# Kernel optimization log

Measured on AMD Instinct MI355X. Metric: run time of the kernel, lower is better.

The kernel has to match this reference:

```python
import jax, jax.numpy as jnp
import numpy as np

RES_UP_RATIO = 0.05   # reserve_up_ratio (mgr.args default)
RES_DN_RATIO = 0.02   # reserve_dn_ratio
REQ_UP_RATIO = 0.02   # system_reserve_up_ratio
REQ_DN_RATIO = 0.02   # system_reserve_dn_ratio


def _build_K(G):
    """Static constraint matrix of the per-timestep LP over x=[P, R_up, R_dn] (n=3G).
    Row 0 is the equality sum(P)=D; remaining rows are <= inequalities."""
    n = 3 * G
    m = 1 + 4 * G + 2
    K = np.zeros((m, n), dtype=np.float32)
    I = np.eye(G, dtype=np.float32)
    K[0, :G] = 1.0                      # sum_g P = D
    r = 1
    K[r:r+G, :G] = I;  K[r:r+G, G:2*G] = I;  r += G      # P + R_up <= pmax
    K[r:r+G, :G] = -I; K[r:r+G, 2*G:3*G] = I; r += G     # -P + R_dn <= -pmin
    K[r:r+G, :G] = I;  r += G                             # P <= pmax
    K[r:r+G, :G] = -I; r += G                             # -P <= -pmin
    K[r, G:2*G] = -1.0; r += 1                            # -sum R_up <= -req_up*D
    K[r, 2*G:3*G] = -1.0                                  # -sum R_dn <= -req_dn*D
    return K


def _solve_da_lp(forecast, pmin, pmax, b, n_iters):
    """Batched PDHG (Chambolle-Pock) solve of all B*T per-timestep LPs.
    Returns P, R_up, R_dn with shape (B, T, G)."""
    B, T = forecast.shape
    G = b.shape[0]
    Knp = _build_K(G)
    L = float(np.linalg.norm(Knp, 2))          # static spectral norm of K
    tau = sigma = 0.9 / L
    K = jnp.asarray(Knp)
    m, n = K.shape
    # objective coefficients over x=[P, R_up, R_dn] (Cost = b*P + c is affine)
    c_obj = jnp.concatenate([b, RES_UP_RATIO * b, RES_DN_RATIO * b])  # (n,)
    # rhs q: (B, T, m)
    q = jnp.concatenate([
        forecast[..., None],
        jnp.broadcast_to(pmax, (B, T, G)),
        jnp.broadcast_to(-pmin, (B, T, G)),
        jnp.broadcast_to(pmax, (B, T, G)),
        jnp.broadcast_to(-pmin, (B, T, G)),
        -REQ_UP_RATIO * forecast[..., None],
        -REQ_DN_RATIO * forecast[..., None],
    ], axis=-1)
    ineq = (jnp.arange(m) > 0)  # row 0 = equality dual (unprojected)

    x0 = jnp.zeros((B, T, n), dtype=forecast.dtype)
    y0 = jnp.zeros((B, T, m), dtype=forecast.dtype)

    def step(carry, _):
        x, y = carry
        x_new = jnp.maximum(x - tau * (c_obj + jnp.einsum('btm,mn->btn', y, K)), 0.0)
        x_bar = 2.0 * x_new - x
        y_new = y + sigma * (jnp.einsum('btn,mn->btm', x_bar, K) - q)
        y_new = jnp.where(ineq, jnp.maximum(y_new, 0.0), y_new)
        return (x_new, y_new), None

    (x, _), _ = jax.lax.scan(step, (x0, y0), None, length=n_iters)
    P = x[..., :G]
    Ru = x[..., G:2*G]
    Rd = x[..., 2*G:3*G]
    return P, Ru, Rd


def setup_inputs() -> dict:
    key = jax.random.key(0)
    k1, k2, k3, k4 = jax.random.split(key, 4)
    G, B, T = 50, 128, 24
    pmax = 100.0 + 400.0 * jax.random.uniform(k1, (G,), dtype=jnp.float32)
    pmin = 0.1 * pmax
    b = 20.0 + 30.0 * jax.random.uniform(k2, (G,), dtype=jnp.float32)
    c = 100.0 * jax.random.uniform(k3, (G,), dtype=jnp.float32)
    lo, hi = jnp.sum(pmin), jnp.sum(pmax)
    # feasible demand: comfortably inside [sum pmin, sum pmax] so reserves exist
    forecast = lo + (0.35 + 0.3 * jax.random.uniform(k4, (B, T), dtype=jnp.float32)) * (hi - lo)
    return {"forecast": forecast, "pmin": pmin, "pmax": pmax, "b": b, "c": c, "n_iters": 300}


def reference(forecast, pmin, pmax, b, c, n_iters):
    P, Ru, Rd = _solve_da_lp(forecast, pmin, pmax, b, n_iters)  # (B,T,G)
    # match torch layout (B, G, T)
    P_DA = jnp.swapaxes(P, 1, 2)
    R_up = jnp.swapaxes(Ru, 1, 2)
    R_dn = jnp.swapaxes(Rd, 1, 2)
    Cost_DA = b[None, :, None] * P_DA + c[None, :, None]
    ru_price = (RES_UP_RATIO * b)[None, :, None]
    rd_price = (RES_DN_RATIO * b)[None, :, None]
    obj = Cost_DA.sum((1, 2)) + (ru_price * R_up).sum((1, 2)) + (rd_price * R_dn).sum((1, 2))
    return (P_DA, R_up, R_dn, obj, Cost_DA)
```

## Files before the change

### kernel.cpp

```cpp
#include <hip/hip_runtime.h>
#include <math.h>

#define G   50
#define T   24
#define B   128
#define NLP (B * T)
#define SZ  (B * G * T)

typedef float v2f __attribute__((ext_vector_type(2)));


__device__ __forceinline__ v2f vmax0(v2f v) {
    v2f z = {0.f, 0.f};
    return __builtin_elementwise_max(v, z);
}

template <int CTRL>
__device__ __forceinline__ float dpp_mov(float x) {
    int r = __builtin_amdgcn_update_dpp(0, __float_as_int(x), CTRL, 0xf, 0xf, true);
    return __int_as_float(r);
}

__device__ __forceinline__ void row_sum3(float& a, float& b, float& c) {
    asm("s_nop 1\n\t"
        "v_add_f32_dpp %0, %0, %0 row_ror:1 row_mask:0xf bank_mask:0xf\n\t"
        "v_add_f32_dpp %1, %1, %1 row_ror:1 row_mask:0xf bank_mask:0xf\n\t"
        "v_add_f32_dpp %2, %2, %2 row_ror:1 row_mask:0xf bank_mask:0xf\n\t"
        "v_add_f32_dpp %0, %0, %0 row_ror:2 row_mask:0xf bank_mask:0xf\n\t"
        "v_add_f32_dpp %1, %1, %1 row_ror:2 row_mask:0xf bank_mask:0xf\n\t"
        "v_add_f32_dpp %2, %2, %2 row_ror:2 row_mask:0xf bank_mask:0xf\n\t"
        "v_add_f32_dpp %0, %0, %0 row_ror:4 row_mask:0xf bank_mask:0xf\n\t"
        "v_add_f32_dpp %1, %1, %1 row_ror:4 row_mask:0xf bank_mask:0xf\n\t"
        "v_add_f32_dpp %2, %2, %2 row_ror:4 row_mask:0xf bank_mask:0xf\n\t"
        "v_add_f32_dpp %0, %0, %0 row_ror:8 row_mask:0xf bank_mask:0xf\n\t"
        "v_add_f32_dpp %1, %1, %1 row_ror:8 row_mask:0xf bank_mask:0xf\n\t"
        "v_add_f32_dpp %2, %2, %2 row_ror:8 row_mask:0xf bank_mask:0xf"
        : "+v"(a), "+v"(b), "+v"(c));
}

__device__ __forceinline__ float row_sum1(float a) {
    a += dpp_mov<0x121>(a);
    a += dpp_mov<0x122>(a);
    a += dpp_mov<0x124>(a);
    a += dpp_mov<0x128>(a);
    return a;
}

__device__ __forceinline__ float half_sum1(float a) {
    a = row_sum1(a);
    float t;
    asm("ds_swizzle_b32 %0, %1 offset:0x401f\n\t"
        "s_waitcnt lgkmcnt(0)"
        : "=&v"(t) : "v"(a));
    return a + t;
}

__global__ __launch_bounds__(64)
void pdhg_lp_kernel(const float* __restrict__ forecast,
                    const float* __restrict__ pmin,
                    const float* __restrict__ pmax,
                    const float* __restrict__ bcost,
                    const float* __restrict__ ccost,
                    const int*   __restrict__ n_iters_p,
                    float* __restrict__ out,
                    float* __restrict__ ws_partial,
                    float tau)
{
    const int lane = threadIdx.x;
    const int l    = lane & 31;
    const int half = lane >> 5;
    const int lp   = blockIdx.x * 2 + half;
    const int b    = lp / T;
    const int t    = lp - b * T;
    const int n_iters = n_iters_p[0];

    const int  g0 = l;
    const int  g1 = l + 32;
    const bool v1 = (l < 18);

    v2f bj  = { bcost[g0], v1 ? bcost[g1] : 0.f };
    v2f cj  = { ccost[g0], v1 ? ccost[g1] : 0.f };
    v2f pmx = { pmax[g0],  v1 ? pmax[g1]  : 0.f };
    v2f pmn = { pmin[g0],  v1 ? pmin[g1]  : 0.f };
    const float f = forecast[lp];

    const float ts  = tau * tau;
    const float BIG = 1e30f;

    v2f tcP  = tau * bj;           if (!v1) tcP.y  = BIG;
    v2f tcRu = (tau * 0.05f) * bj; if (!v1) tcRu.y = BIG;
    v2f tcRd = (tau * 0.02f) * bj; if (!v1) tcRd.y = BIG;
    v2f tspmx = ts * pmx, tspmn = ts * pmn;
    const float tsf   = ts * f;
    const float tsreq = ts * 0.02f * f;

    v2f P = {0,0}, Ru = {0,0}, Rd = {0,0};
    v2f z1 = {0,0}, z2 = {0,0}, z3 = {0,0}, z4 = {0,0};
    float z0 = 0.f, zru = 0.f, zrd = 0.f;

    for (int it = 0; it < n_iters; ++it) {
        v2f z0v  = { z0,  z0  };
        v2f zruv = { zru, zru };
        v2f zrdv = { zrd, zrd };
        v2f gP  = (z1 - z2) + (z3 - z4) + z0v;
        v2f Pn  = vmax0(P  - tcP  - gP);
        v2f Run = vmax0(Ru - tcRu - z1 + zruv);
        v2f Rdn = vmax0(Rd - tcRd - z2 + zrdv);

        v2f Pb  = 2.f * Pn  - P;
        v2f Rub = 2.f * Run - Ru;
        v2f Rdb = 2.f * Rdn - Rd;
        P = Pn; Ru = Run; Rd = Rdn;

        float sP  = Pb.x  + Pb.y;
        float sRu = Rub.x + Rub.y;
        float sRd = Rdb.x + Rdb.y;
        row_sum3(sP, sRu, sRd);

        float xP, xRu, xRd;
        asm("ds_swizzle_b32 %0, %3 offset:0x401f\n\t"
            "ds_swizzle_b32 %1, %4 offset:0x401f\n\t"
            "ds_swizzle_b32 %2, %5 offset:0x401f"
            : "=&v"(xP), "=&v"(xRu), "=&v"(xRd)
            : "v"(sP), "v"(sRu), "v"(sRd));

        z1 = vmax0(z1 + ts * (Pb + Rub) - tspmx);
        z2 = vmax0(z2 + ts * (Rdb - Pb) + tspmn);
        z3 = vmax0(z3 + ts * Pb - tspmx);
        z4 = vmax0(z4 - ts * Pb + tspmn);

        asm("s_waitcnt lgkmcnt(0)" : "+v"(xP), "+v"(xRu), "+v"(xRd));
        sP += xP; sRu += xRu; sRd += xRd;

        z0  = z0 + ts * sP - tsf;
        zru = fmaxf(zru + tsreq - ts * sRu, 0.f);
        zrd = fmaxf(zrd + tsreq - ts * sRd, 0.f);
    }

    const v2f cost = bj * P + cj;
    {
        const int bgt = b * (G * T) + t;
        const int a0 = bgt + g0 * T;
        out[a0] = P.x;  out[SZ + a0] = Ru.x;  out[2*SZ + a0] = Rd.x;  out[3*SZ + B + a0] = cost.x;
        if (v1) {
            const int a1 = bgt + g1 * T;
            out[a1] = P.y;  out[SZ + a1] = Ru.y;  out[2*SZ + a1] = Rd.y;  out[3*SZ + B + a1] = cost.y;
        }
    }

    if (ws_partial) {
        v2f lo = cost + (0.05f * bj) * Ru + (0.02f * bj) * Rd;
        float tot = half_sum1(lo.x + lo.y);
        if (l == 0) ws_partial[lp] = tot;
    }
}

__global__ __launch_bounds__(64)
void obj_final_kernel(const float* __restrict__ ws_partial, float* __restrict__ out)
{
    const int b = blockIdx.x * 64 + threadIdx.x;
    if (b < B) {
        float s = 0.f;
        #pragma unroll
        for (int t = 0; t < T; ++t) s += ws_partial[b * T + t];
        out[3 * SZ + b] = s;
    }
}

__global__ __launch_bounds__(256)
void obj_kernel(const float* __restrict__ bcost, float* __restrict__ out)
{
    const int b = blockIdx.x;
    const float* Ru = out + SZ     + (size_t)b * (G * T);
    const float* Rd = out + 2 * SZ + (size_t)b * (G * T);
    const float* C  = out + 3 * SZ + B + (size_t)b * (G * T);

    float s = 0.f;
    for (int i = threadIdx.x; i < G * T; i += 256) {
        const int g = i / T;
        const float bg = bcost[g];
        s += C[i] + 0.05f * bg * Ru[i] + 0.02f * bg * Rd[i];
    }
    __shared__ float sm[16];
    s = row_sum1(s);
    if ((threadIdx.x & 15) == 0) sm[threadIdx.x >> 4] = s;
    __syncthreads();
    if (threadIdx.x == 0) {
        float tot = 0.f;
        #pragma unroll
        for (int i = 0; i < 16; ++i) tot += sm[i];
        out[3 * SZ + b] = tot;
    }
}

extern "C" void kernel_launch(void* const* d_in, const int* in_sizes, int n_in,
                              void* d_out, int out_size, void* d_ws, size_t ws_size,
                              hipStream_t stream) {
    const float* forecast = (const float*)d_in[0];
    const float* pmin_p   = (const float*)d_in[1];
    const float* pmax_p   = (const float*)d_in[2];
    const float* b_p      = (const float*)d_in[3];
    const float* c_p      = (const float*)d_in[4];
    const int*   niter_p  = (const int*)  d_in[5];
    float* out = (float*)d_out;

    const double L = sqrt((105.0 + sqrt(17.0)) * 0.5);
    const float tau = (float)(0.9 / L);

    const bool use_ws = (ws_size >= (size_t)NLP * sizeof(float));
    float* wsp = use_ws ? (float*)d_ws : nullptr;

    pdhg_lp_kernel<<<NLP / 2, 64, 0, stream>>>(forecast, pmin_p, pmax_p,
                                               b_p, c_p, niter_p, out, wsp, tau);
    if (use_ws) {
        obj_final_kernel<<<(B + 63) / 64, 64, 0, stream>>>(wsp, out);
    } else {
        obj_kernel<<<B, 256, 0, stream>>>(b_p, out);
    }
}
```

Measured before the change: 147.2 us.

## Map one LP per wavefront with full-wave DPP reduction and readlane

Switches from packing two LPs per 64-lane wavefront, with two generators per lane held in float2 vectors, to one LP per wavefront with one generator per lane. Only 50 of the 64 lanes do useful work. The per-iteration sums now use row_bcast DPP steps plus v_readlane into scalar registers, replacing the ds_swizzle exchange that went through the LDS unit and needed a wait on it. The grid doubles, which gives more waves per SIMD to hide the latency of the serial 300-iteration loop. The cost is more total VALU instructions and fewer lanes doing useful work.

```diff
diff --git a/kernel.cpp b/kernel.cpp
--- a/kernel.cpp
+++ b/kernel.cpp
@@ -7,13 +7,6 @@
 #define NLP (B * T)
 #define SZ  (B * G * T)
 
-typedef float v2f __attribute__((ext_vector_type(2)));
-
-
-__device__ __forceinline__ v2f vmax0(v2f v) {
-    v2f z = {0.f, 0.f};
-    return __builtin_elementwise_max(v, z);
-}
 
 template <int CTRL>
 __device__ __forceinline__ float dpp_mov(float x) {
@@ -21,7 +14,16 @@
     return __int_as_float(r);
 }
 
-__device__ __forceinline__ void row_sum3(float& a, float& b, float& c) {
+__device__ __forceinline__ float row_sum1(float a) {
+    a += dpp_mov<0x121>(a);
+    a += dpp_mov<0x122>(a);
+    a += dpp_mov<0x124>(a);
+    a += dpp_mov<0x128>(a);
+    return a;
+}
+
+__device__ __forceinline__ void wave_sum3(float& a, float& b, float& c,
+                                          float& ta, float& tb, float& tc) {
     asm("s_nop 1\n\t"
         "v_add_f32_dpp %0, %0, %0 row_ror:1 row_mask:0xf bank_mask:0xf\n\t"
         "v_add_f32_dpp %1, %1, %1 row_ror:1 row_mask:0xf bank_mask:0xf\n\t"
@@ -34,25 +36,37 @@
         "v_add_f32_dpp %2, %2, %2 row_ror:4 row_mask:0xf bank_mask:0xf\n\t"
         "v_add_f32_dpp %0, %0, %0 row_ror:8 row_mask:0xf bank_mask:0xf\n\t"
         "v_add_f32_dpp %1, %1, %1 row_ror:8 row_mask:0xf bank_mask:0xf\n\t"
-        "v_add_f32_dpp %2, %2, %2 row_ror:8 row_mask:0xf bank_mask:0xf"
-        : "+v"(a), "+v"(b), "+v"(c));
-}
-
-__device__ __forceinline__ float row_sum1(float a) {
-    a += dpp_mov<0x121>(a);
-    a += dpp_mov<0x122>(a);
-    a += dpp_mov<0x124>(a);
-    a += dpp_mov<0x128>(a);
-    return a;
-}
-
-__device__ __forceinline__ float half_sum1(float a) {
-    a = row_sum1(a);
-    float t;
-    asm("ds_swizzle_b32 %0, %1 offset:0x401f\n\t"
-        "s_waitcnt lgkmcnt(0)"
-        : "=&v"(t) : "v"(a));
-    return a + t;
+        "v_add_f32_dpp %2, %2, %2 row_ror:8 row_mask:0xf bank_mask:0xf\n\t"
+        "v_add_f32_dpp %0, %0, %0 row_bcast:15 row_mask:0xa bank_mask:0xf\n\t"
+        "v_add_f32_dpp %1, %1, %1 row_bcast:15 row_mask:0xa bank_mask:0xf\n\t"
+        "v_add_f32_dpp %2, %2, %2 row_bcast:15 row_mask:0xa bank_mask:0xf\n\t"
+        "v_add_f32_dpp %0, %0, %0 row_bcast:31 row_mask:0xc bank_mask:0xf\n\t"
+        "v_add_f32_dpp %1, %1, %1 row_bcast:31 row_mask:0xc bank_mask:0xf\n\t"
+        "v_add_f32_dpp %2, %2, %2 row_bcast:31 row_mask:0xc bank_mask:0xf\n\t"
+        "v_readlane_b32 %3, %0, 63\n\t"
+        "v_readlane_b32 %4, %1, 63\n\t"
+        "v_readlane_b32 %5, %2, 63"
+        : "+v"(a), "+v"(b), "+v"(c), "=s"(ta), "=s"(tb), "=s"(tc));
+}
+
+__device__ __forceinline__ float wave_sum1(float a) {
+    float s;
+    asm("s_nop 1\n\t"
+        "v_add_f32_dpp %0, %0, %0 row_ror:1 row_mask:0xf bank_mask:0xf\n\t"
+        "s_nop 1\n\t"
+        "v_add_f32_dpp %0, %0, %0 row_ror:2 row_mask:0xf bank_mask:0xf\n\t"
+        "s_nop 1\n\t"
+        "v_add_f32_dpp %0, %0, %0 row_ror:4 row_mask:0xf bank_mask:0xf\n\t"
+        "s_nop 1\n\t"
+        "v_add_f32_dpp %0, %0, %0 row_ror:8 row_mask:0xf bank_mask:0xf\n\t"
+        "s_nop 1\n\t"
+        "v_add_f32_dpp %0, %0, %0 row_bcast:15 row_mask:0xa bank_mask:0xf\n\t"
+        "s_nop 1\n\t"
+        "v_add_f32_dpp %0, %0, %0 row_bcast:31 row_mask:0xc bank_mask:0xf\n\t"
+        "s_nop 1\n\t"
+        "v_readlane_b32 %1, %0, 63"
+        : "+v"(a), "=s"(s));
+    return s;
 }
 
 __global__ __launch_bounds__(64)
@@ -67,91 +81,68 @@
                     float tau)
 {
     const int lane = threadIdx.x;
-    const int l    = lane & 31;
-    const int half = lane >> 5;
-    const int lp   = blockIdx.x * 2 + half;
+    const int lp   = blockIdx.x;
     const int b    = lp / T;
     const int t    = lp - b * T;
     const int n_iters = n_iters_p[0];
 
-    const int  g0 = l;
-    const int  g1 = l + 32;
-    const bool v1 = (l < 18);
-
-    v2f bj  = { bcost[g0], v1 ? bcost[g1] : 0.f };
-    v2f cj  = { ccost[g0], v1 ? ccost[g1] : 0.f };
-    v2f pmx = { pmax[g0],  v1 ? pmax[g1]  : 0.f };
-    v2f pmn = { pmin[g0],  v1 ? pmin[g1]  : 0.f };
+    const int  g  = lane;
+    const bool vg = (lane < G);
+
+    const float bj  = vg ? bcost[g] : 0.f;
+    const float cj  = vg ? ccost[g] : 0.f;
+    const float pmx = vg ? pmax[g]  : 0.f;
+    const float pmn = vg ? pmin[g]  : 0.f;
     const float f = forecast[lp];
 
     const float ts  = tau * tau;
     const float BIG = 1e30f;
 
-    v2f tcP  = tau * bj;           if (!v1) tcP.y  = BIG;
-    v2f tcRu = (tau * 0.05f) * bj; if (!v1) tcRu.y = BIG;
-    v2f tcRd = (tau * 0.02f) * bj; if (!v1) tcRd.y = BIG;
-    v2f tspmx = ts * pmx, tspmn = ts * pmn;
+    const float tcP  = vg ? (tau * bj)         : BIG;
+    const float tcRu = vg ? (tau * 0.05f * bj) : BIG;
+    const float tcRd = vg ? (tau * 0.02f * bj) : BIG;
+    const float tspmx = ts * pmx, tspmn = ts * pmn;
     const float tsf   = ts * f;
     const float tsreq = ts * 0.02f * f;
 
-    v2f P = {0,0}, Ru = {0,0}, Rd = {0,0};
-    v2f z1 = {0,0}, z2 = {0,0}, z3 = {0,0}, z4 = {0,0};
+    float P = 0.f, Ru = 0.f, Rd = 0.f;
+    float z1 = 0.f, z2 = 0.f, z3 = 0.f, z4 = 0.f;
     float z0 = 0.f, zru = 0.f, zrd = 0.f;
 
     for (int it = 0; it < n_iters; ++it) {
-        v2f z0v  = { z0,  z0  };
-        v2f zruv = { zru, zru };
-        v2f zrdv = { zrd, zrd };
-        v2f gP  = (z1 - z2) + (z3 - z4) + z0v;
-        v2f Pn  = vmax0(P  - tcP  - gP);
-        v2f Run = vmax0(Ru - tcRu - z1 + zruv);
-        v2f Rdn = vmax0(Rd - tcRd - z2 + zrdv);
-
-        v2f Pb  = 2.f * Pn  - P;
-        v2f Rub = 2.f * Run - Ru;
-        v2f Rdb = 2.f * Rdn - Rd;
+        float gP  = (z1 - z2) + (z3 - z4) + z0;
+        float Pn  = fmaxf(P  - tcP  - gP, 0.f);
+        float Run = fmaxf(Ru - tcRu - (z1 - zru), 0.f);
+        float Rdn = fmaxf(Rd - tcRd - (z2 - zrd), 0.f);
+
+        float Pb  = 2.f * Pn  - P;
+        float Rub = 2.f * Run - Ru;
+        float Rdb = 2.f * Rdn - Rd;
         P = Pn; Ru = Run; Rd = Rdn;
 
-        float sP  = Pb.x  + Pb.y;
-        float sRu = Rub.x + Rub.y;
-        float sRd = Rdb.x + Rdb.y;
-        row_sum3(sP, sRu, sRd);
-
-        float xP, xRu, xRd;
-        asm("ds_swizzle_b32 %0, %3 offset:0x401f\n\t"
-            "ds_swizzle_b32 %1, %4 offset:0x401f\n\t"
-            "ds_swizzle_b32 %2, %5 offset:0x401f"
-            : "=&v"(xP), "=&v"(xRu), "=&v"(xRd)
-            : "v"(sP), "v"(sRu), "v"(sRd));
-
-        z1 = vmax0(z1 + ts * (Pb + Rub) - tspmx);
-        z2 = vmax0(z2 + ts * (Rdb - Pb) + tspmn);
-        z3 = vmax0(z3 + ts * Pb - tspmx);
-        z4 = vmax0(z4 - ts * Pb + tspmn);
-
-        asm("s_waitcnt lgkmcnt(0)" : "+v"(xP), "+v"(xRu), "+v"(xRd));
-        sP += xP; sRu += xRu; sRd += xRd;
-
-        z0  = z0 + ts * sP - tsf;
-        zru = fmaxf(zru + tsreq - ts * sRu, 0.f);
-        zrd = fmaxf(zrd + tsreq - ts * sRd, 0.f);
-    }
-
-    const v2f cost = bj * P + cj;
-    {
-        const int bgt = b * (G * T) + t;
-        const int a0 = bgt + g0 * T;
-        out[a0] = P.x;  out[SZ + a0] = Ru.x;  out[2*SZ + a0] = Rd.x;  out[3*SZ + B + a0] = cost.x;
-        if (v1) {
-            const int a1 = bgt + g1 * T;
-            out[a1] = P.y;  out[SZ + a1] = Ru.y;  out[2*SZ + a1] = Rd.y;  out[3*SZ + B + a1] = cost.y;
-        }
+        float sP = Pb, sRu = Rub, sRd = Rdb;
+        float tP, tRu, tRd;
+        wave_sum3(sP, sRu, sRd, tP, tRu, tRd);
+
+        z1 = fmaxf(z1 + ts * (Pb + Rub) - tspmx, 0.f);
+        z2 = fmaxf(z2 + ts * (Rdb - Pb) + tspmn, 0.f);
+        z3 = fmaxf(z3 + ts * Pb - tspmx, 0.f);
+        z4 = fmaxf(z4 - ts * Pb + tspmn, 0.f);
+        z0  = z0 + ts * tP - tsf;
+        zru = fmaxf(zru + tsreq - ts * tRu, 0.f);
+        zrd = fmaxf(zrd + tsreq - ts * tRd, 0.f);
+    }
+
+    const float cost = bj * P + cj;
+    if (vg) {
+        const int a0 = b * (G * T) + t + g * T;
+        out[a0] = P;  out[SZ + a0] = Ru;  out[2*SZ + a0] = Rd;  out[3*SZ + B + a0] = cost;
     }
 
     if (ws_partial) {
-        v2f lo = cost + (0.05f * bj) * Ru + (0.02f * bj) * Rd;
-        float tot = half_sum1(lo.x + lo.y);
-        if (l == 0) ws_partial[lp] = tot;
+        float lo = cost + (0.05f * bj) * Ru + (0.02f * bj) * Rd;
+        float tot = wave_sum1(lo);
+        if (lane == 0) ws_partial[lp] = tot;
     }
 }
 
@@ -210,8 +201,8 @@
     const bool use_ws = (ws_size >= (size_t)NLP * sizeof(float));
     float* wsp = use_ws ? (float*)d_ws : nullptr;
 
-    pdhg_lp_kernel<<<NLP / 2, 64, 0, stream>>>(forecast, pmin_p, pmax_p,
-                                               b_p, c_p, niter_p, out, wsp, tau);
+    pdhg_lp_kernel<<<NLP, 64, 0, stream>>>(forecast, pmin_p, pmax_p,
+                                           b_p, c_p, niter_p, out, wsp, tau);
     if (use_ws) {
         obj_final_kernel<<<(B + 63) / 64, 64, 0, stream>>>(wsp, out);
     } else {
```

Measured after the change: 166.6 us. 1.13x slower.
